# Kernel tuning notes

Measured on AMD Instinct MI355X. Metric: run time of the kernel, lower is better.

The kernel has to match this reference:

```python
import jax, jax.numpy as jnp
import numpy as np

EMBED_DIM = 1024
NUM_HEADS = 16
HEAD_DIM = EMBED_DIM // NUM_HEADS


def setup_inputs() -> dict:
    key = jax.random.key(0)
    k1, k2, k3, k4, k5 = jax.random.split(key, 5)
    B, S, D = 4, 2048, EMBED_DIM
    scale = 1.0 / np.sqrt(D)
    qkv = jax.random.normal(k1, (B, S, D), dtype=jnp.float32)
    W_in = jax.random.uniform(k2, (D, 3 * D), dtype=jnp.float32, minval=-scale, maxval=scale)
    b_in = jax.random.uniform(k3, (3 * D,), dtype=jnp.float32, minval=-scale, maxval=scale)
    W_out = jax.random.uniform(k4, (D, D), dtype=jnp.float32, minval=-scale, maxval=scale)
    b_out = jax.random.uniform(k5, (D,), dtype=jnp.float32, minval=-scale, maxval=scale)
    return {"qkv": qkv, "W_in": W_in, "b_in": b_in, "W_out": W_out, "b_out": b_out}


def reference(qkv, W_in, b_in, W_out, b_out):
    B, S, D = qkv.shape
    H, hd = NUM_HEADS, HEAD_DIM
    proj = qkv @ W_in + b_in                      # [B, S, 3D]
    q, k, v = jnp.split(proj, 3, axis=-1)         # each [B, S, D]
    # reshape to heads: [B, H, S, hd]
    q = q.reshape(B, S, H, hd).transpose(0, 2, 1, 3)
    k = k.reshape(B, S, H, hd).transpose(0, 2, 1, 3)
    v = v.reshape(B, S, H, hd).transpose(0, 2, 1, 3)
    scores = jnp.einsum('bhqd,bhkd->bhqk', q, k) / jnp.sqrt(jnp.float32(hd))
    attn = jax.nn.softmax(scores, axis=-1)        # dropout=0.0 -> identity
    ctx = jnp.einsum('bhqk,bhkd->bhqd', attn, v)  # [B, H, S, hd]
    ctx = ctx.transpose(0, 2, 1, 3).reshape(B, S, D)
    return ctx @ W_out + b_out
```

## Files before the change

kernel.cpp:

```cpp
#include <hip/hip_runtime.h>


typedef __bf16 bf16;
typedef __bf16 bf16x4 __attribute__((ext_vector_type(4)));
typedef __bf16 bf16x8 __attribute__((ext_vector_type(8)));
typedef float f32x4 __attribute__((ext_vector_type(4)));

typedef const __attribute__((address_space(1))) void* gas1p;
typedef __attribute__((address_space(3))) void* las3p;
#define GLD16(g, l) __builtin_amdgcn_global_load_lds((gas1p)(g), (las3p)(l), 16, 0, 0)

#if __has_builtin(__builtin_amdgcn_exp2f)
#define EXP2(x) __builtin_amdgcn_exp2f(x)
#else
#define EXP2(x) exp2f(x)
#endif

__device__ __forceinline__ f32x4 mfma16(bf16x8 a, bf16x8 b, f32x4 c) {
  return __builtin_amdgcn_mfma_f32_16x16x32_bf16(a, b, c, 0, 0, 0);
}

__global__ void cast_kernel(const float* __restrict__ in, bf16* __restrict__ out, int n) {
  int i = (blockIdx.x * 256 + threadIdx.x) * 4;
  if (i < n) {
    float4 v = *(const float4*)(in + i);
    bf16x4 o;
    o[0] = (bf16)v.x; o[1] = (bf16)v.y; o[2] = (bf16)v.z; o[3] = (bf16)v.w;
    *(bf16x4*)(out + i) = o;
  }
}

__global__ void transpose_cast_kernel(const float* __restrict__ in, bf16* __restrict__ out,
                                      int R, int C) {
  __shared__ float tile[32][33];
  int c0 = blockIdx.x * 32, r0 = blockIdx.y * 32;
  int tx = threadIdx.x, ty = threadIdx.y;
#pragma unroll
  for (int i = 0; i < 4; ++i)
    tile[ty + i * 8][tx] = in[(size_t)(r0 + ty + i * 8) * C + c0 + tx];
  __syncthreads();
#pragma unroll
  for (int i = 0; i < 4; ++i)
    out[(size_t)(c0 + ty + i * 8) * R + r0 + tx] = (bf16)tile[tx][ty + i * 8];
}

__device__ __forceinline__ void stage_tile(const bf16* __restrict__ src, size_t rstride,
                                           int kt, char* dst, int tid) {
#pragma unroll
  for (int i = 0; i < 4; ++i) {
    int chunk = i * 256 + tid;
    int row = chunk >> 3;
    int cs = (chunk & 7) ^ (row & 7);
    GLD16(src + (size_t)row * rstride + kt + cs * 8, dst + chunk * 16);
  }
}

__device__ __forceinline__ void gemm_step(
    const bf16* __restrict__ A, const bf16* __restrict__ B, int m0, int n0,
    const char* ca, const char* cb, char* na, char* nb, int ktn, bool pref,
    int tid, int lane, int quad, int wm, int wn, f32x4 (&acc)[4][4]) {
  if (pref) {
    stage_tile(A + (size_t)m0 * 1024, 1024, ktn, na, tid);
    stage_tile(B + (size_t)n0 * 1024, 1024, ktn, nb, tid);
  }
#pragma unroll
  for (int ks = 0; ks < 2; ++ks) {
    bf16x8 af[4], bfr[4];
#pragma unroll
    for (int t = 0; t < 4; ++t) {
      int ra = wm + t * 16 + (lane & 15);
      af[t] = *(const bf16x8*)(ca + ra * 128 + ((ks * 4 + quad) ^ (ra & 7)) * 16);
      int rb = wn + t * 16 + (lane & 15);
      bfr[t] = *(const bf16x8*)(cb + rb * 128 + ((ks * 4 + quad) ^ (rb & 7)) * 16);
    }
#pragma unroll
    for (int mt = 0; mt < 4; ++mt)
#pragma unroll
      for (int nt = 0; nt < 4; ++nt)
        acc[mt][nt] = mfma16(af[mt], bfr[nt], acc[mt][nt]);
  }
  __syncthreads();
}

__global__ __launch_bounds__(256, 2) void gemm1_kernel(
    const bf16* __restrict__ A, const bf16* __restrict__ Bt, const float* __restrict__ bias,
    bf16* __restrict__ Qo, bf16* __restrict__ Ko, bf16* __restrict__ Vo) {
  __shared__ __align__(16) char sA[2][128 * 64 * 2];
  __shared__ __align__(16) char sB[2][128 * 64 * 2];
  const int tid = threadIdx.x, lane = tid & 63, quad = lane >> 4;
  const int wave = tid >> 6;
  const int m0 = blockIdx.y * 128, n0 = blockIdx.x * 128;
  const int wm = (wave >> 1) * 64, wn = (wave & 1) * 64;
  f32x4 acc[4][4] = {};

  stage_tile(A + (size_t)m0 * 1024, 1024, 0, sA[0], tid);
  stage_tile(Bt + (size_t)n0 * 1024, 1024, 0, sB[0], tid);
  __syncthreads();
  for (int it = 0; it < 16; it += 2) {
    gemm_step(A, Bt, m0, n0, sA[0], sB[0], sA[1], sB[1], (it + 1) * 64, true,
              tid, lane, quad, wm, wn, acc);
    gemm_step(A, Bt, m0, n0, sA[1], sB[1], sA[0], sB[0], (it + 2) * 64, it + 2 < 16,
              tid, lane, quad, wm, wn, acc);
  }

  const int region = n0 >> 10;
#pragma unroll
  for (int nt = 0; nt < 4; ++nt) {
    int n = n0 + wn + nt * 16 + (lane & 15);
    float bv = bias[n];
    int ncol = n & 1023;
    int h = ncol >> 6, d = ncol & 63;
#pragma unroll
    for (int mt = 0; mt < 4; ++mt) {
      int gm = m0 + wm + mt * 16 + quad * 4;
      int bb = gm >> 11, s = gm & 2047;
      if (region == 2) {
        bf16x4 pk;
#pragma unroll
        for (int r = 0; r < 4; ++r) pk[r] = (bf16)(acc[mt][nt][r] + bv);
        *(bf16x4*)(Vo + ((size_t)((bb * 16 + h) * 64 + d)) * 2048 + s) = pk;
      } else {
        bf16* dst = (region == 0) ? Qo : Ko;
        float scl = (region == 0) ? 0.18033688f : 1.0f;
#pragma unroll
        for (int r = 0; r < 4; ++r)
          dst[((size_t)((bb * 16 + h) * 2048) + s + r) * 64 + d] =
              (bf16)((acc[mt][nt][r] + bv) * scl);
      }
    }
  }
}

__global__ __launch_bounds__(256, 2) void flash_kernel(
    const bf16* __restrict__ Q, const bf16* __restrict__ K, const bf16* __restrict__ Vt,
    bf16* __restrict__ ctx) {
  const int n = blockIdx.x;
  const int bh = (n & 7) * 8 + (n >> 6);
  const int qt = (n >> 3) & 7;
  const int b = bh >> 4, h = bh & 15;
  const int tid = threadIdx.x, lane = tid & 63, wave = tid >> 6, quad = lane >> 4;

  __shared__ __align__(16) char sK[2][128 * 64 * 2];
  __shared__ __align__(16) char sV[2][64 * 128 * 2];
  __shared__ __align__(16) char sP[4][64 * 32 * 2];

  const size_t hb = (size_t)bh * 2048 * 64;
  const int q0 = qt * 256;

#pragma unroll
  for (int i = 0; i < 8; ++i) {
    int chunk = i * 256 + tid;
    int row = chunk >> 3;
    int cs = (chunk & 7) ^ (row & 7);
    char* dst = (i < 4) ? (sK[0] + chunk * 16) : (sK[1] + (chunk - 1024) * 16);
    GLD16(Q + hb + (size_t)(q0 + row) * 64 + cs * 8, dst);
  }
  __syncthreads();
  bf16x8 qf[4][2];
#pragma unroll
  for (int j = 0; j < 4; ++j)
#pragma unroll
    for (int ksd = 0; ksd < 2; ++ksd) {
      int row = wave * 64 + j * 16 + (lane & 15);
      const char* src = sK[row >> 7];
      int r128 = row & 127;
      qf[j][ksd] = *(const bf16x8*)(src + r128 * 128 + ((ksd * 4 + quad) ^ (r128 & 7)) * 16);
    }
  __syncthreads();

#pragma unroll
  for (int i = 0; i < 4; ++i) {
    int chunk = i * 256 + tid;
    int row = chunk >> 3;
    int cs = (chunk & 7) ^ (row & 7);
    GLD16(K + hb + (size_t)row * 64 + cs * 8, sK[0] + chunk * 16);
    int vrow = chunk >> 4;
    int vcs = (chunk & 15) ^ (vrow & 7);
    GLD16(Vt + hb + (size_t)vrow * 2048 + vcs * 8, sV[0] + chunk * 16);
  }
  __syncthreads();

  f32x4 ctxa[4][4] = {};
  float l[4] = {0.f, 0.f, 0.f, 0.f};
  char* pw = sP[wave];

  for (int it = 0; it < 16; ++it) {
    const int kv0 = it * 128;
    if (it < 15) {
      char* nk = sK[(it + 1) & 1];
      char* nv = sV[(it + 1) & 1];
#pragma unroll
      for (int i = 0; i < 4; ++i) {
        int chunk = i * 256 + tid;
        int row = chunk >> 3;
        int cs = (chunk & 7) ^ (row & 7);
        GLD16(K + hb + (size_t)(kv0 + 128 + row) * 64 + cs * 8, nk + chunk * 16);
        int vrow = chunk >> 4;
        int vcs = (chunk & 15) ^ (vrow & 7);
        GLD16(Vt + hb + (size_t)vrow * 2048 + kv0 + 128 + vcs * 8, nv + chunk * 16);
      }
    }
    const char* cb = sK[it & 1];
    const char* vb = sV[it & 1];

#pragma unroll
    for (int kq = 0; kq < 4; ++kq) {
      f32x4 st[2][4] = {};
#pragma unroll
      for (int ksd = 0; ksd < 2; ++ksd) {
        bf16x8 kf[2];
#pragma unroll
        for (int ii = 0; ii < 2; ++ii) {
          int row = kq * 32 + ii * 16 + (lane & 15);
          kf[ii] = *(const bf16x8*)(cb + row * 128 + ((ksd * 4 + quad) ^ (row & 7)) * 16);
        }
#pragma unroll
        for (int ii = 0; ii < 2; ++ii)
#pragma unroll
          for (int j = 0; j < 4; ++j)
            st[ii][j] = mfma16(kf[ii], qf[j][ksd], st[ii][j]);
      }
#pragma unroll
      for (int ii = 0; ii < 2; ++ii)
#pragma unroll
        for (int j = 0; j < 4; ++j) {
          f32x4 p;
#pragma unroll
          for (int r = 0; r < 4; ++r) {
            p[r] = EXP2(st[ii][j][r]);
            l[j] += p[r];
          }
          bf16x4 pk;
#pragma unroll
          for (int r = 0; r < 4; ++r) pk[r] = (bf16)p[r];
          int q = j * 16 + (lane & 15);
          int chunk = ii * 2 + (quad >> 1);
          *(bf16x4*)(pw + q * 64 + ((chunk ^ (q & 3)) * 16) + (quad & 1) * 8) = pk;
        }
      bf16x8 pf[4], vf[4];
#pragma unroll
      for (int mt = 0; mt < 4; ++mt) {
        int q = mt * 16 + (lane & 15);
        pf[mt] = *(const bf16x8*)(pw + q * 64 + ((quad ^ (q & 3)) * 16));
      }
#pragma unroll
      for (int nd = 0; nd < 4; ++nd) {
        int row = nd * 16 + (lane & 15);
        vf[nd] = *(const bf16x8*)(vb + row * 256 + (((kq * 4 + quad) ^ (row & 7)) * 16));
      }
#pragma unroll
      for (int mt = 0; mt < 4; ++mt)
#pragma unroll
        for (int nd = 0; nd < 4; ++nd)
          ctxa[mt][nd] = mfma16(pf[mt], vf[nd], ctxa[mt][nd]);
    }
    __syncthreads();
  }

#pragma unroll
  for (int j = 0; j < 4; ++j) {
    l[j] += __shfl_xor(l[j], 16);
    l[j] += __shfl_xor(l[j], 32);
  }
#pragma unroll
  for (int mt = 0; mt < 4; ++mt)
#pragma unroll
    for (int r = 0; r < 4; ++r) {
      float lsh = __shfl(l[mt], quad * 4 + r);
      float rl = __builtin_amdgcn_rcpf(lsh);
      int srow = q0 + wave * 64 + mt * 16 + quad * 4 + r;
#pragma unroll
      for (int nd = 0; nd < 4; ++nd) {
        int col = h * 64 + nd * 16 + (lane & 15);
        ctx[((size_t)(b * 2048 + srow)) * 1024 + col] = (bf16)(ctxa[mt][nd][r] * rl);
      }
    }
}

__global__ __launch_bounds__(256, 2) void gemm2_kernel(
    const bf16* __restrict__ A, const bf16* __restrict__ Bt, const float* __restrict__ bias,
    float* __restrict__ Out) {
  __shared__ __align__(16) char sA[2][128 * 64 * 2];
  __shared__ __align__(16) char sB[2][128 * 64 * 2];
  const int tid = threadIdx.x, lane = tid & 63, quad = lane >> 4;
  const int wave = tid >> 6;
  const int m0 = blockIdx.y * 128, n0 = blockIdx.x * 128;
  const int wm = (wave >> 1) * 64, wn = (wave & 1) * 64;
  f32x4 acc[4][4] = {};

  stage_tile(A + (size_t)m0 * 1024, 1024, 0, sA[0], tid);
  stage_tile(Bt + (size_t)n0 * 1024, 1024, 0, sB[0], tid);
  __syncthreads();
  for (int it = 0; it < 16; it += 2) {
    gemm_step(A, Bt, m0, n0, sA[0], sB[0], sA[1], sB[1], (it + 1) * 64, true,
              tid, lane, quad, wm, wn, acc);
    gemm_step(A, Bt, m0, n0, sA[1], sB[1], sA[0], sB[0], (it + 2) * 64, it + 2 < 16,
              tid, lane, quad, wm, wn, acc);
  }

#pragma unroll
  for (int nt = 0; nt < 4; ++nt) {
    int n = n0 + wn + nt * 16 + (lane & 15);
    float bv = bias[n];
#pragma unroll
    for (int mt = 0; mt < 4; ++mt) {
      int gm = m0 + wm + mt * 16 + quad * 4;
#pragma unroll
      for (int r = 0; r < 4; ++r)
        Out[(size_t)(gm + r) * 1024 + n] = acc[mt][nt][r] + bv;
    }
  }
}

extern "C" void kernel_launch(void* const* d_in, const int* in_sizes, int n_in,
                              void* d_out, int out_size, void* d_ws, size_t ws_size,
                              hipStream_t stream) {
  const float* qkv   = (const float*)d_in[0];
  const float* W_in  = (const float*)d_in[1];
  const float* b_in  = (const float*)d_in[2];
  const float* W_out = (const float*)d_in[3];
  const float* b_out = (const float*)d_in[4];
  float* out = (float*)d_out;

  bf16* Xb    = (bf16*)d_ws;
  bf16* WtIn  = Xb + 8388608;
  bf16* WtOut = WtIn + 3145728;
  bf16* Qb    = WtOut + 1048576;
  bf16* Kb    = Qb + 8388608;
  bf16* Vtb   = Kb + 8388608;
  bf16* Ctx   = Xb;

  cast_kernel<<<8192, 256, 0, stream>>>(qkv, Xb, 8388608);
  transpose_cast_kernel<<<dim3(96, 32), dim3(32, 8), 0, stream>>>(W_in, WtIn, 1024, 3072);
  transpose_cast_kernel<<<dim3(32, 32), dim3(32, 8), 0, stream>>>(W_out, WtOut, 1024, 1024);
  gemm1_kernel<<<dim3(24, 64), 256, 0, stream>>>(Xb, WtIn, b_in, Qb, Kb, Vtb);
  flash_kernel<<<512, 256, 0, stream>>>(Qb, Kb, Vtb, Ctx);
  gemm2_kernel<<<dim3(8, 64), 256, 0, stream>>>(Ctx, WtOut, b_out, out);
}
```

Before: 264.2 us.

## Fuse prep kernels into one launch and remap GEMM blocks for XCD locality

Merges the activation cast and both weight transpose-casts into a single prep kernel, removing two launches. Both GEMM kernels now use a 1D grid whose block index is remapped so each of the 8 XCDs handles a contiguous band of 8 M-tiles, walking N-tiles in an order meant to improve L2 reuse of A rows within an XCD. The mapping assumes round-robin dispatch of blocks across 8 XCDs and fixed grid sizes (64 M-tiles).

```diff
diff --git a/kernel.cpp b/kernel.cpp
--- a/kernel.cpp
+++ b/kernel.cpp
@@ -20,21 +20,28 @@
   return __builtin_amdgcn_mfma_f32_16x16x32_bf16(a, b, c, 0, 0, 0);
 }
 
-__global__ void cast_kernel(const float* __restrict__ in, bf16* __restrict__ out, int n) {
-  int i = (blockIdx.x * 256 + threadIdx.x) * 4;
-  if (i < n) {
-    float4 v = *(const float4*)(in + i);
+__global__ void prep_kernel(const float* __restrict__ qkv, bf16* __restrict__ Xb,
+                            const float* __restrict__ W_in, bf16* __restrict__ WtIn,
+                            const float* __restrict__ W_out, bf16* __restrict__ WtOut) {
+  __shared__ float tile[32][33];
+  int blk = blockIdx.x, tid = threadIdx.x;
+  if (blk < 8192) {
+    int i = (blk * 256 + tid) * 4;
+    float4 v = *(const float4*)(qkv + i);
     bf16x4 o;
     o[0] = (bf16)v.x; o[1] = (bf16)v.y; o[2] = (bf16)v.z; o[3] = (bf16)v.w;
-    *(bf16x4*)(out + i) = o;
-  }
-}
-
-__global__ void transpose_cast_kernel(const float* __restrict__ in, bf16* __restrict__ out,
-                                      int R, int C) {
-  __shared__ float tile[32][33];
-  int c0 = blockIdx.x * 32, r0 = blockIdx.y * 32;
-  int tx = threadIdx.x, ty = threadIdx.y;
+    *(bf16x4*)(Xb + i) = o;
+    return;
+  }
+  const float* in; bf16* out; int R, C, c0, r0;
+  if (blk < 11264) {
+    int t = blk - 8192; in = W_in; out = WtIn; R = 1024; C = 3072;
+    c0 = (t % 96) * 32; r0 = (t / 96) * 32;
+  } else {
+    int t = blk - 11264; in = W_out; out = WtOut; R = 1024; C = 1024;
+    c0 = (t % 32) * 32; r0 = (t / 32) * 32;
+  }
+  int tx = tid & 31, ty = tid >> 5;
 #pragma unroll
   for (int i = 0; i < 4; ++i)
     tile[ty + i * 8][tx] = in[(size_t)(r0 + ty + i * 8) * C + c0 + tx];
@@ -89,7 +96,8 @@
   __shared__ __align__(16) char sB[2][128 * 64 * 2];
   const int tid = threadIdx.x, lane = tid & 63, quad = lane >> 4;
   const int wave = tid >> 6;
-  const int m0 = blockIdx.y * 128, n0 = blockIdx.x * 128;
+  const int id = blockIdx.x, xcd = id & 7, local = id >> 3;
+  const int m0 = (xcd * 8 + (local & 7)) * 128, n0 = (local >> 3) * 128;
   const int wm = (wave >> 1) * 64, wn = (wave & 1) * 64;
   f32x4 acc[4][4] = {};
 
@@ -284,7 +292,8 @@
   __shared__ __align__(16) char sB[2][128 * 64 * 2];
   const int tid = threadIdx.x, lane = tid & 63, quad = lane >> 4;
   const int wave = tid >> 6;
-  const int m0 = blockIdx.y * 128, n0 = blockIdx.x * 128;
+  const int id = blockIdx.x, xcd = id & 7, local = id >> 3;
+  const int m0 = (xcd * 8 + (local & 7)) * 128, n0 = (local >> 3) * 128;
   const int wm = (wave >> 1) * 64, wn = (wave & 1) * 64;
   f32x4 acc[4][4] = {};
 
@@ -330,10 +339,8 @@
   bf16* Vtb   = Kb + 8388608;
   bf16* Ctx   = Xb;
 
-  cast_kernel<<<8192, 256, 0, stream>>>(qkv, Xb, 8388608);
-  transpose_cast_kernel<<<dim3(96, 32), dim3(32, 8), 0, stream>>>(W_in, WtIn, 1024, 3072);
-  transpose_cast_kernel<<<dim3(32, 32), dim3(32, 8), 0, stream>>>(W_out, WtOut, 1024, 1024);
-  gemm1_kernel<<<dim3(24, 64), 256, 0, stream>>>(Xb, WtIn, b_in, Qb, Kb, Vtb);
+  prep_kernel<<<12288, 256, 0, stream>>>(qkv, Xb, W_in, WtIn, W_out, WtOut);
+  gemm1_kernel<<<1536, 256, 0, stream>>>(Xb, WtIn, b_in, Qb, Kb, Vtb);
   flash_kernel<<<512, 256, 0, stream>>>(Qb, Kb, Vtb, Ctx);
-  gemm2_kernel<<<dim3(8, 64), 256, 0, stream>>>(Ctx, WtOut, b_out, out);
-}
+  gemm2_kernel<<<512, 256, 0, stream>>>(Ctx, WtOut, b_out, out);
+}
```

Result: faster. 251.3 us (-4.9%).
